# Optimization experiments

Hardware: AMD Instinct MI355X
Metric: run time of the kernel (lower is better)

The kernel has to match this reference:

```python
import jax, jax.numpy as jnp
import numpy as np

N_NODES = 100000
N_EDGES = 1600000
HID = 32


def gcn_conv(x, W, b, src, dst, num_nodes):
    # PyG GCNConv: h = X W; out = D^{-1/2}(A+I)D^{-1/2} h + b
    # (self loops already appended to src/dst by caller)
    h = x @ W
    deg = jax.ops.segment_sum(jnp.ones_like(dst, dtype=h.dtype), dst,
                              num_segments=num_nodes)
    dinv = jnp.where(deg > 0, jax.lax.rsqrt(deg), 0.0)
    norm = dinv[src] * dinv[dst]                      # [E+N]
    msg = h[src] * norm[:, None]                      # gather + scale
    out = jax.ops.segment_sum(msg, dst, num_segments=num_nodes)  # scatter-add
    return out + b


def setup_inputs() -> dict:
    key = jax.random.key(0)
    ks = jax.random.split(key, 12)
    x = jax.random.normal(ks[0], (N_NODES, 2), dtype=jnp.float32)
    edge_index = jax.random.randint(ks[1], (2, N_EDGES), 0, N_NODES,
                                    dtype=jnp.int32)
    s = 0.2  # small init scale
    return {
        "x": x,
        "edge_index": edge_index,
        "fc1_W": jax.random.normal(ks[2], (2, HID), jnp.float32) * s,
        "fc1_b": jnp.zeros((HID,), jnp.float32),
        "c1_W": jax.random.normal(ks[3], (HID, HID), jnp.float32) * s,
        "c1_b": jnp.zeros((HID,), jnp.float32),
        "c2_W": jax.random.normal(ks[4], (HID, HID), jnp.float32) * s,
        "c2_b": jnp.zeros((HID,), jnp.float32),
        "c3_W": jax.random.normal(ks[5], (HID, HID), jnp.float32) * s,
        "c3_b": jnp.zeros((HID,), jnp.float32),
        "fc2_W": jax.random.normal(ks[6], (HID, HID), jnp.float32) * s,
        "fc2_b": jnp.zeros((HID,), jnp.float32),
        "fc3_W": jax.random.normal(ks[7], (HID, 1), jnp.float32) * s,
        "fc3_b": jnp.zeros((1,), jnp.float32),
    }


def reference(x, edge_index, fc1_W, fc1_b, c1_W, c1_b, c2_W, c2_b,
              c3_W, c3_b, fc2_W, fc2_b, fc3_W, fc3_b):
    num_nodes = x.shape[0]
    loop = jnp.arange(num_nodes, dtype=edge_index.dtype)
    src = jnp.concatenate([edge_index[0], loop])  # add self loops
    dst = jnp.concatenate([edge_index[1], loop])
    h = jax.nn.relu(x @ fc1_W + fc1_b)
    h = jax.nn.relu(gcn_conv(h, c1_W, c1_b, src, dst, num_nodes))
    h = jax.nn.relu(gcn_conv(h, c2_W, c2_b, src, dst, num_nodes))
    h = jax.nn.relu(gcn_conv(h, c3_W, c3_b, src, dst, num_nodes))
    h = jax.nn.relu(h @ fc2_W + fc2_b)
    return h @ fc3_W + fc3_b
```

## Files before the change

kernel.cpp:

```cpp
#include <hip/hip_runtime.h>

#define NN 100000
#define NE 1600000
#define HID 32
#define NBK 98
#define CAP 18000
#define CHUNK 4096

__global__ void partA_kernel(const int* __restrict__ src, const int* __restrict__ dst,
                             int* __restrict__ bktcur, int* __restrict__ bedges) {
    __shared__ int hist[NBK];
    __shared__ int lofs[NBK];
    int t = threadIdx.x;
    int base = blockIdx.x * CHUNK;
    int end = min(base + CHUNK, NE);
    if (t < NBK) hist[t] = 0;
    __syncthreads();
    for (int e = base + t; e < end; e += 256)
        atomicAdd(&hist[dst[e] >> 10], 1);
    __syncthreads();
    if (t < NBK) lofs[t] = hist[t] ? atomicAdd(&bktcur[t], hist[t]) : 0;
    __syncthreads();
    for (int e = base + t; e < end; e += 256) {
        int d = dst[e], s = src[e];
        int b = d >> 10;
        int rel = atomicAdd(&lofs[b], 1);
        if (rel < CAP) bedges[b * CAP + rel] = (s << 10) | (d & 1023);
    }
}

__global__ __launch_bounds__(512) void bucket_csr_kernel(
        const int* __restrict__ bedges, const int* __restrict__ bktcur,
        float* __restrict__ dinv, int* __restrict__ srcidx,
        int* __restrict__ rbeg, int* __restrict__ rend) {
    __shared__ int ldeg[1024];
    __shared__ int lcur[1024];
    __shared__ int wsum[512];
    int b = blockIdx.x, t = threadIdx.x;
    int ebeg = b * CAP;
    int cnt = min(bktcur[b], CAP);
    int eend = ebeg + cnt;
    ldeg[t] = 0; ldeg[t + 512] = 0;
    __syncthreads();
    for (int e = ebeg + t; e < eend; e += 512)
        atomicAdd(&ldeg[bedges[e] & 1023], 1);
    __syncthreads();
    int a0 = ldeg[2 * t], a1 = ldeg[2 * t + 1];
    int s = a0 + a1;
    wsum[t] = s;
    __syncthreads();
    for (int off = 1; off < 512; off <<= 1) {
        int x = (t >= off) ? wsum[t - off] : 0;
        __syncthreads();
        wsum[t] += x;
        __syncthreads();
    }
    int excl = wsum[t] - s;
    lcur[2 * t] = excl;
    lcur[2 * t + 1] = excl + a0;
    int n = (b << 10) + 2 * t;
    if (n < NN) {
        rbeg[n] = ebeg + excl;
        rend[n] = ebeg + excl + a0;
        dinv[n] = rsqrtf((float)(a0 + 1));
    }
    if (n + 1 < NN) {
        rbeg[n + 1] = ebeg + excl + a0;
        rend[n + 1] = ebeg + excl + a0 + a1;
        dinv[n + 1] = rsqrtf((float)(a1 + 1));
    }
    __syncthreads();
    for (int e = ebeg + t; e < eend; e += 512) {
        int w = bedges[e];
        int pos = atomicAdd(&lcur[w & 1023], 1);
        srcidx[ebeg + pos] = (unsigned)w >> 10;
    }
}

__global__ void fc1_kernel(const float* __restrict__ x, const float* __restrict__ W,
                           const float* __restrict__ b, const float* __restrict__ dinv,
                           float* __restrict__ hs) {
    int gid = blockIdx.x * blockDim.x + threadIdx.x;
    int n = gid >> 5, j = gid & 31;
    float v = x[2 * n] * W[j] + x[2 * n + 1] * W[HID + j] + b[j];
    hs[gid] = fmaxf(v, 0.f) * dinv[n];
}

template <bool OUTSCALE>
__global__ void conv_fused_kernel(const float* __restrict__ hs_in,
                                  const int* __restrict__ rbeg,
                                  const int* __restrict__ rend,
                                  const int* __restrict__ srcidx,
                                  const float* __restrict__ dinv,
                                  const float* __restrict__ W,
                                  const float* __restrict__ bias,
                                  float* __restrict__ hs_out) {
    __shared__ float wl[HID * HID];
    __shared__ float agg[8][HID];
    int tid = threadIdx.x;
    int base8 = blockIdx.x * 8;
#pragma unroll
    for (int i = 0; i < 4; ++i) wl[tid + 256 * i] = W[tid + 256 * i];
    int wave = tid >> 6, lane = tid & 63;
    int g = lane >> 3;
    int l = lane & 7;
#pragma unroll
    for (int rep = 0; rep < 2; ++rep) {
        int ln = wave * 2 + rep;
        int n = base8 + ln;
        int beg = rbeg[n], end = rend[n];
        float4 acc0 = make_float4(0.f, 0.f, 0.f, 0.f);
        float4 acc1 = make_float4(0.f, 0.f, 0.f, 0.f);
        int e = beg + g;
        for (; e + 8 < end; e += 16) {
            int s0 = srcidx[e];
            int s1 = srcidx[e + 8];
            float4 v0 = *(const float4*)&hs_in[(s0 << 5) + (l << 2)];
            float4 v1 = *(const float4*)&hs_in[(s1 << 5) + (l << 2)];
            acc0.x += v0.x; acc0.y += v0.y; acc0.z += v0.z; acc0.w += v0.w;
            acc1.x += v1.x; acc1.y += v1.y; acc1.z += v1.z; acc1.w += v1.w;
        }
        if (e < end) {
            int s0 = srcidx[e];
            float4 v0 = *(const float4*)&hs_in[(s0 << 5) + (l << 2)];
            acc0.x += v0.x; acc0.y += v0.y; acc0.z += v0.z; acc0.w += v0.w;
        }
        acc0.x += acc1.x; acc0.y += acc1.y; acc0.z += acc1.z; acc0.w += acc1.w;
#pragma unroll
        for (int m = 8; m < 64; m <<= 1) {
            acc0.x += __shfl_xor(acc0.x, m);
            acc0.y += __shfl_xor(acc0.y, m);
            acc0.z += __shfl_xor(acc0.z, m);
            acc0.w += __shfl_xor(acc0.w, m);
        }
        if (g == 0) {
            float4 self = *(const float4*)&hs_in[(n << 5) + (l << 2)];
            float dv = dinv[n];
            float4 r;
            r.x = (acc0.x + self.x) * dv;
            r.y = (acc0.y + self.y) * dv;
            r.z = (acc0.z + self.z) * dv;
            r.w = (acc0.w + self.w) * dv;
            *(float4*)&agg[ln][l << 2] = r;
        }
    }
    __syncthreads();
    int ln = tid >> 5, j = tid & 31;
    int n = base8 + ln;
    float v = 0.f;
#pragma unroll
    for (int k = 0; k < HID; ++k) v += agg[ln][k] * wl[k * HID + j];
    v = fmaxf(v + bias[j], 0.f);
    if (OUTSCALE) v *= dinv[n];
    hs_out[(n << 5) + j] = v;
}

__global__ void fc23_kernel(const float* __restrict__ h, const float* __restrict__ W2,
                            const float* __restrict__ b2, const float* __restrict__ W3,
                            const float* __restrict__ b3, float* __restrict__ out) {
    __shared__ float wl[HID * HID];
    __shared__ float hsl[256];
    int tid = threadIdx.x;
    int base = blockIdx.x * 256;
#pragma unroll
    for (int i = 0; i < 4; ++i) wl[tid + 256 * i] = W2[tid + 256 * i];
    hsl[tid] = h[base + tid];
    __syncthreads();
    int ln = tid >> 5, j = tid & 31;
    float v = 0.f;
#pragma unroll
    for (int k = 0; k < HID; ++k) v += hsl[ln * HID + k] * wl[k * HID + j];
    v = fmaxf(v + b2[j], 0.f);
    float p = v * W3[j];
#pragma unroll
    for (int m = 16; m; m >>= 1) p += __shfl_xor(p, m);
    if (j == 0) out[(base >> 5) + ln] = p + b3[0];
}

extern "C" void kernel_launch(void* const* d_in, const int* in_sizes, int n_in,
                              void* d_out, int out_size, void* d_ws, size_t ws_size,
                              hipStream_t stream) {
    const float* x     = (const float*)d_in[0];
    const int*   ei    = (const int*)d_in[1];
    const float* fc1_W = (const float*)d_in[2];
    const float* fc1_b = (const float*)d_in[3];
    const float* c1_W  = (const float*)d_in[4];
    const float* c1_b  = (const float*)d_in[5];
    const float* c2_W  = (const float*)d_in[6];
    const float* c2_b  = (const float*)d_in[7];
    const float* c3_W  = (const float*)d_in[8];
    const float* c3_b  = (const float*)d_in[9];
    const float* fc2_W = (const float*)d_in[10];
    const float* fc2_b = (const float*)d_in[11];
    const float* fc3_W = (const float*)d_in[12];
    const float* fc3_b = (const float*)d_in[13];

    const int* src = ei;
    const int* dst = ei + NE;

    float* ws     = (float*)d_ws;
    float* dinv   = ws;
    float* hA     = ws + NN;
    float* hB     = hA + NN * HID;
    int*   srcidx = (int*)(hB + NN * HID);
    int*   rbeg   = srcidx + NBK * CAP;
    int*   rend   = rbeg + NN;
    int*   bktcur = rend + NN;
    int*   bedges = (int*)hA;

    float* out = (float*)d_out;

    const int B = 256;
    const int gNH = (NN * HID) / B;
    const int gPart = (NE + CHUNK - 1) / CHUNK;

    hipMemsetAsync(bktcur, 0, NBK * sizeof(int), stream);
    partA_kernel<<<gPart, B, 0, stream>>>(src, dst, bktcur, bedges);
    bucket_csr_kernel<<<NBK, 512, 0, stream>>>(bedges, bktcur, dinv, srcidx, rbeg, rend);

    fc1_kernel<<<gNH, B, 0, stream>>>(x, fc1_W, fc1_b, dinv, hA);

    conv_fused_kernel<true><<<gNH, B, 0, stream>>>(hA, rbeg, rend, srcidx, dinv, c1_W, c1_b, hB);
    conv_fused_kernel<true><<<gNH, B, 0, stream>>>(hB, rbeg, rend, srcidx, dinv, c2_W, c2_b, hA);
    conv_fused_kernel<false><<<gNH, B, 0, stream>>>(hA, rbeg, rend, srcidx, dinv, c3_W, c3_b, hB);

    fc23_kernel<<<gNH, B, 0, stream>>>(hB, fc2_W, fc2_b, fc3_W, fc3_b, out);
}
```

Measured before the change: 203.5 us.

## Use 256-node buckets and fuse fc1 into bucket CSR build

Shrinks destination buckets from 1024 to 256 nodes, giving 391 CSR-build blocks instead of 98 so more CUs work on that phase. The fc1 linear layer is folded into the CSR kernel so it can use the freshly computed dinv from shared memory, removing one launch and a dinv reread. partA now caches dst in shared memory so it is read from global memory only once. Per-bucket capacity drops to 4608 slots, which adds overflow risk for unusually dense node ranges, and the bucket staging buffer moves to hB so it does not collide with the fc1 output.

Measured after the change: 192.5 us. -5.4%, faster.

```diff
diff --git a/kernel.cpp b/kernel.cpp
--- a/kernel.cpp
+++ b/kernel.cpp
@@ -3,87 +3,105 @@
 #define NN 100000
 #define NE 1600000
 #define HID 32
-#define NBK 98
-#define CAP 18000
+#define NBK 391
+#define CAP 4608
 #define CHUNK 4096
 
-__global__ void partA_kernel(const int* __restrict__ src, const int* __restrict__ dst,
-                             int* __restrict__ bktcur, int* __restrict__ bedges) {
+__global__ __launch_bounds__(256) void partA_kernel(
+        const int* __restrict__ src, const int* __restrict__ dst,
+        int* __restrict__ bktcur, int* __restrict__ bedges) {
+    __shared__ int cache[CHUNK];
     __shared__ int hist[NBK];
     __shared__ int lofs[NBK];
     int t = threadIdx.x;
     int base = blockIdx.x * CHUNK;
-    int end = min(base + CHUNK, NE);
-    if (t < NBK) hist[t] = 0;
-    __syncthreads();
-    for (int e = base + t; e < end; e += 256)
-        atomicAdd(&hist[dst[e] >> 10], 1);
-    __syncthreads();
-    if (t < NBK) lofs[t] = hist[t] ? atomicAdd(&bktcur[t], hist[t]) : 0;
-    __syncthreads();
-    for (int e = base + t; e < end; e += 256) {
-        int d = dst[e], s = src[e];
-        int b = d >> 10;
-        int rel = atomicAdd(&lofs[b], 1);
-        if (rel < CAP) bedges[b * CAP + rel] = (s << 10) | (d & 1023);
-    }
-}
-
-__global__ __launch_bounds__(512) void bucket_csr_kernel(
+    for (int i = t; i < NBK; i += 256) hist[i] = 0;
+    __syncthreads();
+    for (int i = t; i < CHUNK; i += 256) {
+        int e = base + i;
+        if (e < NE) {
+            int d = dst[e];
+            cache[i] = d;
+            atomicAdd(&hist[d >> 8], 1);
+        }
+    }
+    __syncthreads();
+    for (int i = t; i < NBK; i += 256)
+        lofs[i] = hist[i] ? atomicAdd(&bktcur[i], hist[i]) : 0;
+    __syncthreads();
+    for (int i = t; i < CHUNK; i += 256) {
+        int e = base + i;
+        if (e < NE) {
+            int d = cache[i];
+            int s = src[e];
+            int b = d >> 8;
+            int rel = atomicAdd(&lofs[b], 1);
+            if (rel < CAP) bedges[b * CAP + rel] = (s << 8) | (d & 255);
+        }
+    }
+}
+
+__global__ __launch_bounds__(256) void bucket_csr_fc1_kernel(
         const int* __restrict__ bedges, const int* __restrict__ bktcur,
-        float* __restrict__ dinv, int* __restrict__ srcidx,
-        int* __restrict__ rbeg, int* __restrict__ rend) {
-    __shared__ int ldeg[1024];
-    __shared__ int lcur[1024];
-    __shared__ int wsum[512];
+        const float* __restrict__ x, const float* __restrict__ W1,
+        const float* __restrict__ b1, float* __restrict__ dinv,
+        int* __restrict__ srcidx, int* __restrict__ rbeg, int* __restrict__ rend,
+        float* __restrict__ hs) {
+    __shared__ int ldeg[256];
+    __shared__ int lcur[256];
+    __shared__ int wsum[256];
+    __shared__ float sdinv[256];
+    __shared__ float xs[512];
+    __shared__ float wb[96];
     int b = blockIdx.x, t = threadIdx.x;
     int ebeg = b * CAP;
     int cnt = min(bktcur[b], CAP);
-    int eend = ebeg + cnt;
-    ldeg[t] = 0; ldeg[t + 512] = 0;
-    __syncthreads();
-    for (int e = ebeg + t; e < eend; e += 512)
-        atomicAdd(&ldeg[bedges[e] & 1023], 1);
-    __syncthreads();
-    int a0 = ldeg[2 * t], a1 = ldeg[2 * t + 1];
-    int s = a0 + a1;
-    wsum[t] = s;
-    __syncthreads();
-    for (int off = 1; off < 512; off <<= 1) {
-        int x = (t >= off) ? wsum[t - off] : 0;
+    int n0 = b << 8;
+    ldeg[t] = 0;
+    if (t < 96) wb[t] = (t < 64) ? W1[t] : b1[t - 64];
+    for (int i = t; i < 512; i += 256) {
+        int gi = 2 * n0 + i;
+        xs[i] = (gi < 2 * NN) ? x[gi] : 0.f;
+    }
+    __syncthreads();
+    for (int e = t; e < cnt; e += 256)
+        atomicAdd(&ldeg[bedges[ebeg + e] & 255], 1);
+    __syncthreads();
+    int a = ldeg[t];
+    wsum[t] = a;
+    __syncthreads();
+    for (int off = 1; off < 256; off <<= 1) {
+        int xv = (t >= off) ? wsum[t - off] : 0;
         __syncthreads();
-        wsum[t] += x;
+        wsum[t] += xv;
         __syncthreads();
     }
-    int excl = wsum[t] - s;
-    lcur[2 * t] = excl;
-    lcur[2 * t + 1] = excl + a0;
-    int n = (b << 10) + 2 * t;
+    int excl = wsum[t] - a;
+    lcur[t] = excl;
+    float dv = rsqrtf((float)(a + 1));
+    sdinv[t] = dv;
+    int n = n0 + t;
     if (n < NN) {
         rbeg[n] = ebeg + excl;
-        rend[n] = ebeg + excl + a0;
-        dinv[n] = rsqrtf((float)(a0 + 1));
-    }
-    if (n + 1 < NN) {
-        rbeg[n + 1] = ebeg + excl + a0;
-        rend[n + 1] = ebeg + excl + a0 + a1;
-        dinv[n + 1] = rsqrtf((float)(a1 + 1));
-    }
-    __syncthreads();
-    for (int e = ebeg + t; e < eend; e += 512) {
-        int w = bedges[e];
-        int pos = atomicAdd(&lcur[w & 1023], 1);
-        srcidx[ebeg + pos] = (unsigned)w >> 10;
-    }
-}
-
-__global__ void fc1_kernel(const float* __restrict__ x, const float* __restrict__ W,
-                           const float* __restrict__ b, const float* __restrict__ dinv,
-                           float* __restrict__ hs) {
-    int gid = blockIdx.x * blockDim.x + threadIdx.x;
-    int n = gid >> 5, j = gid & 31;
-    float v = x[2 * n] * W[j] + x[2 * n + 1] * W[HID + j] + b[j];
-    hs[gid] = fmaxf(v, 0.f) * dinv[n];
+        rend[n] = ebeg + excl + a;
+        dinv[n] = dv;
+    }
+    __syncthreads();
+    for (int e = t; e < cnt; e += 256) {
+        int w = bedges[ebeg + e];
+        int pos = atomicAdd(&lcur[w & 255], 1);
+        srcidx[ebeg + pos] = (unsigned)w >> 8;
+    }
+    int j = t & 31;
+#pragma unroll
+    for (int r = 0; r < 32; ++r) {
+        int ln = (t >> 5) + (r << 3);
+        int nn = n0 + ln;
+        if (nn < NN) {
+            float v = xs[2 * ln] * wb[j] + xs[2 * ln + 1] * wb[32 + j] + wb[64 + j];
+            hs[(nn << 5) + j] = fmaxf(v, 0.f) * sdinv[ln];
+        }
+    }
 }
 
 template <bool OUTSCALE>
@@ -206,7 +224,7 @@
     int*   rbeg   = srcidx + NBK * CAP;
     int*   rend   = rbeg + NN;
     int*   bktcur = rend + NN;
-    int*   bedges = (int*)hA;
+    int*   bedges = (int*)hB;
 
     float* out = (float*)d_out;
 
@@ -216,9 +234,8 @@
 
     hipMemsetAsync(bktcur, 0, NBK * sizeof(int), stream);
     partA_kernel<<<gPart, B, 0, stream>>>(src, dst, bktcur, bedges);
-    bucket_csr_kernel<<<NBK, 512, 0, stream>>>(bedges, bktcur, dinv, srcidx, rbeg, rend);
-
-    fc1_kernel<<<gNH, B, 0, stream>>>(x, fc1_W, fc1_b, dinv, hA);
+    bucket_csr_fc1_kernel<<<NBK, B, 0, stream>>>(bedges, bktcur, x, fc1_W, fc1_b,
+                                                 dinv, srcidx, rbeg, rend, hA);
 
     conv_fused_kernel<true><<<gNH, B, 0, stream>>>(hA, rbeg, rend, srcidx, dinv, c1_W, c1_b, hB);
     conv_fused_kernel<true><<<gNH, B, 0, stream>>>(hB, rbeg, rend, srcidx, dinv, c2_W, c2_b, hA);
```
